# Kernel optimization log

Measured on AMD Instinct MI355X. Metric: run time of the kernel, lower is better.

The kernel has to match this reference:

```python
import jax, jax.numpy as jnp
import numpy as np

H = 300   # hidden_size
B = 2048  # number of graphs
L = 64    # max atoms per graph


def _ragged():
    sizes = 32 + (np.arange(B) % 33)          # sizes in [32, 64], deterministic
    starts = np.concatenate([[0], np.cumsum(sizes)[:-1]])
    N = int(sizes.sum())                       # 98273
    seg_id = np.repeat(np.arange(B), sizes)    # graph id per global node row
    offset = np.arange(N) - starts[seg_id]     # local position within graph
    return sizes, starts, N, seg_id, offset


def setup_inputs() -> dict:
    key = jax.random.key(0)
    sizes, starts, N, seg_id, offset = _ragged()
    ks = jax.random.split(key, 10)
    s = 1.0 / np.sqrt(H)
    u = lambda k, shp: jax.random.uniform(k, shp, jnp.float32, -s, s)
    return {
        "node": jax.random.normal(ks[0], (N, H), jnp.float32),
        "bias": u(ks[1], (H,)),
        "W_ih_f": u(ks[2], (3 * H, H)), "W_hh_f": u(ks[3], (3 * H, H)),
        "b_ih_f": u(ks[4], (3 * H,)), "b_hh_f": u(ks[5], (3 * H,)),
        "W_ih_b": u(ks[6], (3 * H, H)), "W_hh_b": u(ks[7], (3 * H, H)),
        "b_ih_b": u(ks[8], (3 * H,)), "b_hh_b": u(ks[9], (3 * H,)),
        "starts": jnp.asarray(starts, jnp.int32),
        "sizes": jnp.asarray(sizes, jnp.int32),
        "seg_id": jnp.asarray(seg_id, jnp.int32),
        "offset": jnp.asarray(offset, jnp.int32),
    }


def _gru_dir(x, h0, W_ih, W_hh, b_ih, b_hh, reverse):
    # x: [B, L, H], h0: [B, H]; torch nn.GRU cell math, one direction
    xp = jnp.einsum('blh,gh->blg', x, W_ih) + b_ih  # [B, L, 3H]

    def step(h, xt):
        gh = h @ W_hh.T + b_hh
        i_r, i_z, i_n = jnp.split(xt, 3, axis=-1)
        h_r, h_z, h_n = jnp.split(gh, 3, axis=-1)
        r = jax.nn.sigmoid(i_r + h_r)
        z = jax.nn.sigmoid(i_z + h_z)
        n = jnp.tanh(i_n + r * h_n)
        h_new = (1.0 - z) * n + z * h
        return h_new, h_new

    _, ys = jax.lax.scan(step, h0, jnp.swapaxes(xp, 0, 1), reverse=reverse)
    return jnp.swapaxes(ys, 0, 1)  # [B, L, H], time-aligned to input


def reference(node, bias, W_ih_f, W_hh_f, b_ih_f, b_hh_f,
              W_ih_b, W_hh_b, b_ih_b, b_hh_b,
              starts, sizes, seg_id, offset):
    N = node.shape[0]
    message = jax.nn.relu(node + bias)                       # [N, H]

    l_idx = jnp.arange(L)
    mask = l_idx[None, :] < sizes[:, None]                   # [B, L] valid positions
    idx = jnp.clip(starts[:, None] + l_idx[None, :], 0, N - 1)

    # pack: zero-padded per-graph message batch [B, L, H]
    padded = jnp.where(mask[..., None], message[idx], 0.0)
    # per-graph max-pool of raw hidden (node) -> h0 for both GRU directions
    hpool = jnp.max(jnp.where(mask[..., None], node[idx], -jnp.inf), axis=1)

    out_f = _gru_dir(padded, hpool, W_ih_f, W_hh_f, b_ih_f, b_hh_f, reverse=False)
    out_b = _gru_dir(padded, hpool, W_ih_b, W_hh_b, b_ih_b, b_hh_b, reverse=True)
    cur = jnp.concatenate([out_f, out_b], axis=-1)           # [B, L, 2H]

    # unpad back to flat node order
    unpad = cur[seg_id, offset]                              # [N, 2H]
    head = jnp.concatenate([message[:1], message[:1]], axis=1)  # [1, 2H]
    return jnp.concatenate([head, unpad], axis=0)            # [N+1, 2H]
```

## Files before the change

kernel.cpp:

```cpp
#include <hip/hip_runtime.h>
#include <math.h>

#define Hc 300
#define Ld 64
#define GB 16
#define GBF 16
#define KT 10
#define NQ 20
#define NT 60
#define PERDIR (2*2*KT*NT*64)
#define TOTF   (2*PERDIR)
#define NCW 10
#define NTH 768

typedef _Float16 f16x8 __attribute__((ext_vector_type(8)));
typedef float f32x4 __attribute__((ext_vector_type(4)));
typedef unsigned int u32;

#define MFMA16(a,b,c) __builtin_amdgcn_mfma_f32_16x16x32_f16(a,b,c,0,0,0)
#define RBAR() do { __builtin_amdgcn_sched_barrier(0); __builtin_amdgcn_s_barrier(); __builtin_amdgcn_sched_barrier(0); } while (0)

__global__ __launch_bounds__(256) void k_prep(
    const float* __restrict__ Wih_f, const float* __restrict__ Whh_f,
    const float* __restrict__ Wih_b, const float* __restrict__ Whh_b,
    const float* __restrict__ bih_f, const float* __restrict__ bhh_f,
    const float* __restrict__ bih_b, const float* __restrict__ bhh_b,
    const float* __restrict__ node, const float* __restrict__ bias,
    f16x8* __restrict__ Bfrag, float* __restrict__ bcomb, float* __restrict__ out)
{
  int gid = blockIdx.x*256 + threadIdx.x;
  if (gid < TOTF) {
    int lane = gid & 63;
    int s = gid >> 6;
    int nt = s % NT;  s /= NT;
    int kt = s % KT;  s /= KT;
    int term = s & 1; s >>= 1;
    int gemm = s & 1; s >>= 1;
    int dir  = s;
    int sec = nt / NQ, qq = nt - sec*NQ;
    int c = qq*16 + (lane & 15);
    int row = sec*Hc + c;
    const float* W = dir ? (gemm ? Whh_b : Wih_b) : (gemm ? Whh_f : Wih_f);
    f16x8 v;
#pragma unroll
    for (int e = 0; e < 8; ++e) {
      int k = kt*32 + (lane>>4)*8 + e;
      float wv = (c < Hc && k < Hc) ? W[row*Hc + k] : 0.f;
      _Float16 hi = (_Float16)wv;
      v[e] = term ? (_Float16)(wv - (float)hi) : hi;
    }
    Bfrag[gid] = v;
    return;
  }
  int i = gid - TOTF;
  if (i < 2560) {
    int dir = i / 1280; int r = i - dir*1280;
    int buf = r / 320, c = r - buf*320;
    const float* bih = dir ? bih_b : bih_f;
    const float* bhh = dir ? bhh_b : bhh_f;
    float v = 0.f;
    if (c < Hc) {
      if (buf == 0) v = bih[c] + bhh[c];
      else if (buf == 1) v = bih[Hc+c] + bhh[Hc+c];
      else if (buf == 2) v = bih[2*Hc+c];
      else v = bhh[2*Hc+c];
    }
    bcomb[i] = v;
    return;
  }
  i -= 2560;
  if (i < 600) {
    int c = (i < Hc) ? i : i - Hc;
    out[i] = fmaxf(node[c] + bias[c], 0.f);
  }
}

__device__ __forceinline__ u32 f32_to_hl(float v) {
  union { _Float16 f; unsigned short u; } a, b;
  a.f = (_Float16)v;
  b.f = (_Float16)(v - (float)a.f);
  return (u32)a.u | ((u32)b.u << 16);
}

__device__ __forceinline__ float ntl1(const float* p) {
  return __builtin_nontemporal_load(p);
}
__device__ __forceinline__ f32x4 ntl4(const float* p) {
  return __builtin_nontemporal_load((const f32x4*)p);
}

__device__ __forceinline__ void gll16(const void* g, void* l) {
  __builtin_amdgcn_global_load_lds(
      (const __attribute__((address_space(1))) u32*)g,
      (__attribute__((address_space(3))) u32*)l, 16, 0, 0);
}

__device__ __forceinline__ void afh_write(u32 (&buf)[2][KT][256],
                                          int l15, int g, int cE, u32 p, int lane) {
  u32 qv = (u32)__builtin_amdgcn_ds_bpermute((lane ^ 1) << 2, (int)p);
  int kt = cE >> 5;
  int dw = ((((cE >> 3) & 3) << 4) + g) * 4 + ((cE & 7) >> 1);
  if ((l15 & 1) == 0) buf[0][kt][dw] = (p & 0xFFFFu) | (qv << 16);
  else                buf[1][kt][dw] = (qv >> 16) | (p & 0xFFFF0000u);
}

__device__ __forceinline__ float sigf(float x) {
  return __builtin_amdgcn_rcpf(1.f + __expf(-x));
}
__device__ __forceinline__ float tanhfast(float x) {
  return 1.f - 2.f * __builtin_amdgcn_rcpf(__expf(2.f * x) + 1.f);
}

__global__ __launch_bounds__(640) void k_xp(
    const float* __restrict__ node, const float* __restrict__ bias,
    const f16x8* __restrict__ Bfrag, float* __restrict__ xp, int Nrows)
{
  __shared__ __align__(16) u32 AfX[2][4][KT][256];
  int tid = threadIdx.x, w = tid >> 6, lane = tid & 63;
  int l15 = lane & 15, l4 = lane >> 4;
  int r0 = blockIdx.x * 64;

  int k8 = w*32 + (l4 << 3);
  float bb[8];
#pragma unroll
  for (int e = 0; e < 8; ++e) bb[e] = 0.f;
  if (k8 + 8 <= Hc) {
    f32x4 a = *(const f32x4*)&bias[k8];
    f32x4 b = *(const f32x4*)&bias[k8+4];
#pragma unroll
    for (int e = 0; e < 4; ++e) { bb[e] = a[e]; bb[e+4] = b[e]; }
  } else if (k8 < Hc) {
    f32x4 a = *(const f32x4*)&bias[k8];
#pragma unroll
    for (int e = 0; e < 4; ++e) bb[e] = a[e];
  }

#pragma unroll
  for (int mt = 0; mt < 4; ++mt) {
    int row = r0 + mt*16 + l15;
    float xv[8];
#pragma unroll
    for (int e = 0; e < 8; ++e) xv[e] = 0.f;
    if (row < Nrows) {
      const float* rp = node + (size_t)row * Hc + k8;
      if (k8 + 8 <= Hc) {
        f32x4 a = ntl4(rp);
        f32x4 b = ntl4(rp + 4);
#pragma unroll
        for (int e = 0; e < 4; ++e) {
          xv[e]   = fmaxf(a[e] + bb[e],   0.f);
          xv[e+4] = fmaxf(b[e] + bb[e+4], 0.f);
        }
      } else if (k8 < Hc) {
        f32x4 a = ntl4(rp);
#pragma unroll
        for (int e = 0; e < 4; ++e) xv[e] = fmaxf(a[e] + bb[e], 0.f);
      }
    }
    f16x8 vh, vl;
#pragma unroll
    for (int e = 0; e < 8; ++e) {
      vh[e] = (_Float16)xv[e];
      vl[e] = (_Float16)(xv[e] - (float)vh[e]);
    }
    *(f16x8*)&AfX[0][mt][w][lane*4] = vh;
    *(f16x8*)&AfX[1][mt][w][lane*4] = vl;
  }
  __syncthreads();

  int qv0 = w, qv1 = w + 10;
  int c0 = qv0*16 + l15, c1 = qv1*16 + l15;
  const f32x4 zz = {0.f, 0.f, 0.f, 0.f};

#pragma unroll 1
  for (int dir = 0; dir < 2; ++dir) {
    const f16x8* Bxh = Bfrag + (size_t)dir * PERDIR;

#pragma unroll 1
    for (int qi = 0; qi < 2; ++qi) {
      int qv = qi ? qv1 : qv0;
      int c  = qi ? c1  : c0;
      f32x4 acc[3][4];
#pragma unroll
      for (int sec = 0; sec < 3; ++sec)
#pragma unroll
        for (int mt = 0; mt < 4; ++mt) acc[sec][mt] = zz;

#pragma unroll 2
      for (int kt = 0; kt < KT; ++kt) {
        f16x8 axh[4], axl[4];
#pragma unroll
        for (int mt = 0; mt < 4; ++mt) {
          axh[mt] = *(const f16x8*)&AfX[0][mt][kt][lane*4];
          axl[mt] = *(const f16x8*)&AfX[1][mt][kt][lane*4];
        }
#pragma unroll
        for (int sec = 0; sec < 3; ++sec) {
          int nt = sec*NQ + qv;
          f16x8 bh = Bxh[(kt*NT + nt)*64 + lane];
#pragma unroll
          for (int mt = 0; mt < 4; ++mt) {
            acc[sec][mt] = MFMA16(axh[mt], bh, acc[sec][mt]);
            acc[sec][mt] = MFMA16(axl[mt], bh, acc[sec][mt]);
          }
        }
      }
      if (c < 304) {
#pragma unroll
        for (int sec = 0; sec < 3; ++sec)
#pragma unroll
          for (int mt = 0; mt < 4; ++mt)
#pragma unroll
            for (int j = 0; j < 4; ++j) {
              int row = r0 + mt*16 + (l4<<2) + j;
              if (row < Nrows)
                __builtin_nontemporal_store(acc[sec][mt][j],
                    &xp[((size_t)row*2 + dir)*912 + sec*304 + c]);
            }
      }
    }
  }
}

__global__ __launch_bounds__(NTH) void k_rec(
    const float* __restrict__ node,
    const f16x8* __restrict__ Bfrag, const float* __restrict__ bcomb,
    const float* __restrict__ xp,
    const int* __restrict__ starts, const int* __restrict__ sizes,
    float* __restrict__ out)
{
  __shared__ __align__(16) u32 Bbuf[4][7680];
  __shared__ __align__(16) u32 AfH[2][KT][256];
  __shared__ int sst[16], ssz[16];

  int bid = blockIdx.x;
  int dir = (bid & 7) >= 4;
  int tslot = (bid & 3) + (bid >> 3) * 4;
  int g0 = tslot * GB;

  int tid = threadIdx.x;
  int w = tid >> 6, lane = tid & 63;
  int l15 = lane & 15, l4 = lane >> 4;

  if (tid < 16) { sst[tid] = starts[g0 + tid]; ssz[tid] = sizes[g0 + tid]; }

  const f16x8* Bhh = Bfrag + (size_t)dir * PERDIR + 2*KT*NT*64;
  const f32x4 zz = {0.f, 0.f, 0.f, 0.f};

  bool prod = (w >= NCW);
  int pw = w - NCW;

  int qv0 = w, qv1 = w + 10;
  int c0 = qv0*16 + l15, c1 = qv1*16 + l15;

  const float* bc = bcomb + dir*1280;
  float bcr[2], bcz[2], bci[2], bch[2];
  float hreg0[4], hreg1[4];

#define PISSUE(U) { \
    int kt_ = (U) >> 1, hf_ = (U) & 1; \
    char* sb_ = ((char*)&Bbuf[0][0]) + ((U) & 3) * 30720; \
    _Pragma("unroll") \
    for (int ff = 0; ff < 15; ++ff) { \
      int fi_ = pw*15 + ff; \
      int q3_ = fi_ / 3; \
      int sec_ = fi_ - 3*q3_; \
      const f16x8* gs_ = Bhh + ((size_t)(kt_*NT + sec_*NQ + hf_*10 + q3_))*64 + lane; \
      gll16((const void*)gs_, (void*)(sb_ + fi_*1024)); \
    } }

  if (prod) {
    PISSUE(0) PISSUE(1) PISSUE(2)
    asm volatile("s_waitcnt vmcnt(30)" ::: "memory");
  } else {
    bcr[0] = bc[c0];       bcr[1] = bc[c1];
    bcz[0] = bc[320 + c0]; bcz[1] = bc[320 + c1];
    bci[0] = bc[640 + c0]; bci[1] = bc[640 + c1];
    bch[0] = bc[960 + c0]; bch[1] = bc[960 + c1];
  }
  asm volatile("s_waitcnt lgkmcnt(0)" ::: "memory");
  RBAR();

  if (!prod) {
#pragma unroll
    for (int j = 0; j < 4; ++j) {
      int g = (l4<<2) + j;
      int st = sst[g], sz = ssz[g];
      float m0 = -1e30f, m1 = 0.f;
      for (int i = 0; i < sz; ++i)
        m0 = fmaxf(m0, ntl1(&node[(size_t)(st + i) * Hc + c0]));
      if (c1 < Hc) {
        m1 = -1e30f;
        for (int i = 0; i < sz; ++i)
          m1 = fmaxf(m1, ntl1(&node[(size_t)(st + i) * Hc + c1]));
      }
      hreg0[j] = m0;
      hreg1[j] = m1;
      afh_write(AfH, l15, g, c0 & ~1, f32_to_hl(m0), lane);
      afh_write(AfH, l15, g, c1 & ~1, f32_to_hl(m1), lane);
    }
  }
  asm volatile("s_waitcnt lgkmcnt(0)" ::: "memory");
  RBAR();

#pragma unroll 1
  for (int t = 0; t < Ld; ++t) {
    int time = dir ? (Ld-1-t) : t;

    float xvv0[3][4], xvv1[3][4];
    if (!prod) {
#pragma unroll
      for (int j = 0; j < 4; ++j) {
        int g = (l4<<2) + j;
        bool v = (time < ssz[g]);
        const float* xb = xp + ((size_t)(sst[g] + time)*2 + dir)*912 + c0;
#pragma unroll
        for (int sec = 0; sec < 3; ++sec)
          xvv0[sec][j] = v ? ntl1(xb + sec*304) : 0.f;
        bool v1 = (c1 < 304) && v;
        const float* xb1 = xp + ((size_t)(sst[g] + time)*2 + dir)*912 + c1;
#pragma unroll
        for (int sec = 0; sec < 3; ++sec)
          xvv1[sec][j] = v1 ? ntl1(xb1 + sec*304) : 0.f;
      }
    }

    f32x4 ha0[3] = { zz, zz, zz };
    f32x4 ha1[3] = { zz, zz, zz };

#pragma unroll 1
    for (int kt = 0; kt < KT; ++kt) {
      if (prod) {
        int u3 = 2*kt + 3; if (u3 >= 20) u3 -= 20;
        PISSUE(u3)
        asm volatile("s_waitcnt vmcnt(30)" ::: "memory");
      } else {
        const char* bbase = (const char*)&Bbuf[0][0] + ((2*kt) & 3)*30720 + lane*16;
        f16x8 ah = *(const f16x8*)&AfH[0][kt][lane*4];
        f16x8 al = *(const f16x8*)&AfH[1][kt][lane*4];
#pragma unroll
        for (int sec = 0; sec < 3; ++sec) {
          f16x8 b0 = *(const f16x8*)(bbase + (w*3 + sec)*1024);
          ha0[sec] = MFMA16(ah, b0, ha0[sec]);
          ha0[sec] = MFMA16(al, b0, ha0[sec]);
        }
      }
      RBAR();

      if (prod) {
        int u4 = 2*kt + 4; if (u4 >= 20) u4 -= 20;
        PISSUE(u4)
        asm volatile("s_waitcnt vmcnt(30)" ::: "memory");
      } else {
        const char* bbase = (const char*)&Bbuf[0][0] + ((2*kt+1) & 3)*30720 + lane*16;
        f16x8 ah = *(const f16x8*)&AfH[0][kt][lane*4];
        f16x8 al = *(const f16x8*)&AfH[1][kt][lane*4];
#pragma unroll
        for (int sec = 0; sec < 3; ++sec) {
          f16x8 b1 = *(const f16x8*)(bbase + (w*3 + sec)*1024);
          ha1[sec] = MFMA16(ah, b1, ha1[sec]);
          ha1[sec] = MFMA16(al, b1, ha1[sec]);
        }
      }
      RBAR();
    }

    if (!prod) {
#pragma unroll
      for (int j = 0; j < 4; ++j) {
        int g = (l4<<2) + j;
        float rr = sigf(ha0[0][j] + xvv0[0][j] + bcr[0]);
        float zi = sigf(ha0[1][j] + xvv0[1][j] + bcz[0]);
        float nn = tanhfast(xvv0[2][j] + bci[0] + rr * (ha0[2][j] + bch[0]));
        float h_ = (1.f - zi) * nn + zi * hreg0[j];
        hreg0[j] = h_;
        if (time < ssz[g])
          __builtin_nontemporal_store(h_,
              &out[(size_t)(1 + sst[g] + time)*600 + dir*Hc + c0]);
        afh_write(AfH, l15, g, c0 & ~1, f32_to_hl(h_), lane);

        float rr1 = sigf(ha1[0][j] + xvv1[0][j] + bcr[1]);
        float zi1 = sigf(ha1[1][j] + xvv1[1][j] + bcz[1]);
        float nn1 = tanhfast(xvv1[2][j] + bci[1] + rr1 * (ha1[2][j] + bch[1]));
        float h1 = (1.f - zi1) * nn1 + zi1 * hreg1[j];
        if (c1 >= Hc) h1 = 0.f;
        hreg1[j] = h1;
        if (c1 < Hc && time < ssz[g])
          __builtin_nontemporal_store(h1,
              &out[(size_t)(1 + sst[g] + time)*600 + dir*Hc + c1]);
        afh_write(AfH, l15, g, c1 & ~1, f32_to_hl(h1), lane);
      }
    }
    asm volatile("s_waitcnt lgkmcnt(0)" ::: "memory");
    RBAR();
  }
#undef PISSUE
}

__global__ __launch_bounds__(640) void k_rec_fb(
    const float* __restrict__ node, const float* __restrict__ bias,
    const f16x8* __restrict__ Bfrag, const float* __restrict__ bcomb,
    const int* __restrict__ starts, const int* __restrict__ sizes,
    float* __restrict__ out)
{
  __shared__ __align__(16) u32 AfX[2][4][KT][256];
  __shared__ __align__(16) u32 AfH[2][2][KT][256];
  __shared__ int sst[GBF], ssz[GBF];

  int bid = blockIdx.x;
  int dir = (bid & 7) >= 4;
  int tslot = (bid & 3) + (bid >> 3) * 4;
  int g0 = tslot * GBF;

  int tid = threadIdx.x;
  int w = tid >> 6, lane = tid & 63;
  int l15 = lane & 15, l4 = lane >> 4;

  if (tid < GBF) { sst[tid] = starts[g0 + tid]; ssz[tid] = sizes[g0 + tid]; }
  __syncthreads();

  int qv[2] = { w, w + 10 };
  int cq[2] = { qv[0]*16 + l15, qv[1]*16 + l15 };

  const float* bc = bcomb + dir*1280;
  float bcr[2], bcz[2], bci[2], bch[2];
#pragma unroll
  for (int qi = 0; qi < 2; ++qi) {
    int c = cq[qi];
    bcr[qi] = bc[c]; bcz[qi] = bc[320 + c]; bci[qi] = bc[640 + c]; bch[qi] = bc[960 + c];
  }
  int stj[4], szj[4];
#pragma unroll
  for (int j = 0; j < 4; ++j) { stj[j] = sst[(l4<<2)+j]; szj[j] = ssz[(l4<<2)+j]; }
  int stG = sst[l15], szG = ssz[l15];

  const f16x8* Bd  = Bfrag + (size_t)dir * PERDIR;
  const f16x8* Bxh = Bd;
  const f16x8* Bxl = Bd + KT*NT*64;
  const f16x8* Bhh = Bd + 2*KT*NT*64;
  const f16x8* Bhl = Bd + 3*KT*NT*64;
  const f32x4 zz = {0.f, 0.f, 0.f, 0.f};

  int k8 = w*32 + (l4<<3);
  float bb[8];
#pragma unroll
  for (int e = 0; e < 8; ++e) bb[e] = 0.f;
  if (k8 + 8 <= Hc) {
    f32x4 a = *(const f32x4*)&bias[k8];
    f32x4 b = *(const f32x4*)&bias[k8+4];
#pragma unroll
    for (int e = 0; e < 4; ++e) { bb[e] = a[e]; bb[e+4] = b[e]; }
  } else if (k8 < Hc) {
    f32x4 a = *(const f32x4*)&bias[k8];
#pragma unroll
    for (int e = 0; e < 4; ++e) bb[e] = a[e];
  }

  float hreg[2][4];
#pragma unroll
  for (int qi = 0; qi < 2; ++qi) {
    int c = cq[qi];
#pragma unroll
    for (int j = 0; j < 4; ++j) {
      float m = 0.f;
      if (c < Hc) {
        m = -1e30f;
        int st = stj[j], sz = szj[j];
        for (int i = 0; i < sz; ++i)
          m = fmaxf(m, node[(size_t)(st + i) * Hc + c]);
      }
      hreg[qi][j] = m;
      afh_write(AfH[0], l15, (l4<<2)+j, c & ~1, f32_to_hl(m), lane);
    }
  }

#define HSTEPF(S) { \
    constexpr int CUR = (S)&1; \
    constexpr int NXT = CUR^1; \
    f32x4 ha[2][3]; \
    _Pragma("unroll") \
    for (int qi = 0; qi < 2; ++qi) { ha[qi][0] = zz; ha[qi][1] = zz; ha[qi][2] = zz; } \
    _Pragma("unroll 2") \
    for (int kt = 0; kt < KT; ++kt) { \
      f16x8 ahh = *(const f16x8*)&AfH[CUR][0][kt][lane*4]; \
      f16x8 ahl = *(const f16x8*)&AfH[CUR][1][kt][lane*4]; \
      _Pragma("unroll") \
      for (int qi = 0; qi < 2; ++qi) { \
        _Pragma("unroll") \
        for (int sec = 0; sec < 3; ++sec) { \
          int nt = sec*NQ + qv[qi]; \
          f16x8 bh = Bhh[(kt*NT + nt)*64 + lane]; \
          f16x8 bl = Bhl[(kt*NT + nt)*64 + lane]; \
          ha[qi][sec] = MFMA16(ahh, bh, ha[qi][sec]); \
          ha[qi][sec] = MFMA16(ahh, bl, ha[qi][sec]); \
          ha[qi][sec] = MFMA16(ahl, bh, ha[qi][sec]); \
        } \
      } \
    } \
    int tt = 4*T + (S); \
    int time = dir ? (Ld-1-tt) : tt; \
    _Pragma("unroll") \
    for (int qi = 0; qi < 2; ++qi) { \
      int c = cq[qi]; \
      _Pragma("unroll") \
      for (int j = 0; j < 4; ++j) { \
        float rp_ = ha[qi][0][j] + xa[qi][0][S][j] + bcr[qi]; \
        float zp_ = ha[qi][1][j] + xa[qi][1][S][j] + bcz[qi]; \
        float r_ = 1.f/(1.f + __expf(-rp_)); \
        float z_ = 1.f/(1.f + __expf(-zp_)); \
        float n_ = tanhf(xa[qi][2][S][j] + bci[qi] + r_*(ha[qi][2][j] + bch[qi])); \
        float h_ = (1.f - z_)*n_ + z_*hreg[qi][j]; \
        if (c >= Hc) h_ = 0.f; \
        hreg[qi][j] = h_; \
        if (c < Hc && time < szj[j]) \
          out[(size_t)(1 + stj[j] + time)*600 + dir*Hc + c] = h_; \
        afh_write(AfH[NXT], l15, (l4<<2)+j, c & ~1, f32_to_hl(h_), lane); \
      } \
    } \
    __syncthreads(); \
  }

#pragma unroll 1
  for (int T = 0; T < Ld/4; ++T) {
#pragma unroll
    for (int s = 0; s < 4; ++s) {
      int tt = 4*T + s;
      int time = dir ? (Ld-1-tt) : tt;
      float xv[8];
#pragma unroll
      for (int e = 0; e < 8; ++e) xv[e] = 0.f;
      if (time < szG) {
        const float* rp = node + (size_t)(stG + time) * Hc + k8;
        if (k8 + 8 <= Hc) {
          f32x4 a = *(const f32x4*)rp;
          f32x4 b = *(const f32x4*)(rp + 4);
#pragma unroll
          for (int e = 0; e < 4; ++e) {
            xv[e]   = fmaxf(a[e] + bb[e],   0.f);
            xv[e+4] = fmaxf(b[e] + bb[e+4], 0.f);
          }
        } else if (k8 < Hc) {
          f32x4 a = *(const f32x4*)rp;
#pragma unroll
          for (int e = 0; e < 4; ++e) xv[e] = fmaxf(a[e] + bb[e], 0.f);
        }
      }
      f16x8 vh, vl;
#pragma unroll
      for (int e = 0; e < 8; ++e) {
        vh[e] = (_Float16)xv[e];
        vl[e] = (_Float16)(xv[e] - (float)vh[e]);
      }
      *(f16x8*)&AfX[0][s][w][lane*4] = vh;
      *(f16x8*)&AfX[1][s][w][lane*4] = vl;
    }
    __syncthreads();

    f32x4 xa[2][3][4];
#pragma unroll
    for (int qi = 0; qi < 2; ++qi)
#pragma unroll
      for (int sec = 0; sec < 3; ++sec)
#pragma unroll
        for (int mt = 0; mt < 4; ++mt) xa[qi][sec][mt] = zz;

#pragma unroll 1
    for (int kt = 0; kt < KT; ++kt) {
      f16x8 axh[4], axl[4];
#pragma unroll
      for (int mt = 0; mt < 4; ++mt) {
        axh[mt] = *(const f16x8*)&AfX[0][mt][kt][lane*4];
        axl[mt] = *(const f16x8*)&AfX[1][mt][kt][lane*4];
      }
#pragma unroll
      for (int qi = 0; qi < 2; ++qi) {
#pragma unroll
        for (int sec = 0; sec < 3; ++sec) {
          int nt = sec*NQ + qv[qi];
          f16x8 bh = Bxh[(kt*NT + nt)*64 + lane];
          f16x8 bl = Bxl[(kt*NT + nt)*64 + lane];
#pragma unroll
          for (int mt = 0; mt < 4; ++mt) {
            xa[qi][sec][mt] = MFMA16(axh[mt], bh, xa[qi][sec][mt]);
            xa[qi][sec][mt] = MFMA16(axh[mt], bl, xa[qi][sec][mt]);
            xa[qi][sec][mt] = MFMA16(axl[mt], bh, xa[qi][sec][mt]);
          }
        }
      }
    }

    HSTEPF(0)
    HSTEPF(1)
    HSTEPF(2)
    HSTEPF(3)
  }
#undef HSTEPF
}

extern "C" void kernel_launch(void* const* d_in, const int* in_sizes, int n_in,
                              void* d_out, int out_size, void* d_ws, size_t ws_size,
                              hipStream_t stream) {
  const float* node  = (const float*)d_in[0];
  const float* bias  = (const float*)d_in[1];
  const float* Wih_f = (const float*)d_in[2];
  const float* Whh_f = (const float*)d_in[3];
  const float* bih_f = (const float*)d_in[4];
  const float* bhh_f = (const float*)d_in[5];
  const float* Wih_b = (const float*)d_in[6];
  const float* Whh_b = (const float*)d_in[7];
  const float* bih_b = (const float*)d_in[8];
  const float* bhh_b = (const float*)d_in[9];
  const int* starts  = (const int*)d_in[10];
  const int* sizes   = (const int*)d_in[11];

  int ngr = in_sizes[10];
  int N = in_sizes[0] / Hc;

  float* out = (float*)d_out;
  f16x8* Bfrag = (f16x8*)d_ws;
  float* bcomb = (float*)((char*)d_ws + (size_t)TOTF*16);
  size_t xp_off = (size_t)TOTF*16 + 2560*4;
  size_t need = xp_off + (size_t)N * 1824 * 4;

  int prep_threads = TOTF + 2560 + 600;
  hipLaunchKernelGGL(k_prep, dim3((prep_threads + 255)/256), dim3(256), 0, stream,
                     Wih_f, Whh_f, Wih_b, Whh_b, bih_f, bhh_f, bih_b, bhh_b,
                     node, bias, Bfrag, bcomb, out);

  if (ws_size >= need && (ngr % GB) == 0) {
    float* xp = (float*)((char*)d_ws + xp_off);
    int nxb = (N + 63) / 64;
    hipLaunchKernelGGL(k_xp, dim3(nxb), dim3(640), 0, stream,
                       node, bias, Bfrag, xp, N);
    int ntile = ngr / GB;
    hipLaunchKernelGGL(k_rec, dim3(2*ntile), dim3(NTH), 0, stream,
                       node, Bfrag, bcomb, xp, starts, sizes, out);
  } else {
    int ntilef = ngr / GBF;
    hipLaunchKernelGGL(k_rec_fb, dim3(2*ntilef), dim3(640), 0, stream,
                       node, bias, Bfrag, bcomb, starts, sizes, out);
  }
}
```

Baseline: 1.365 ms.

## Restructure recurrent weight streaming into a 7-slot per-gate ring buffer

The W_hh streaming in the recurrent kernel moves from 4 half-k-tile buffers to a 7-slot ring with one slot per gate section of a k-tile, so 30 sub-waves run per timestep instead of 20. Each slot holds only the 19 column quads that are actually needed, which skips loading and multiplying the padded 20th quad. The producer waves keep more loads in flight (up to 6 slots ahead) with per-wave vmcnt thresholds. The cost is more barriers per timestep and tighter coupling to exact vmcnt counts.

```diff
diff --git a/kernel.cpp b/kernel.cpp
--- a/kernel.cpp
+++ b/kernel.cpp
@@ -12,6 +12,8 @@
 #define TOTF   (2*PERDIR)
 #define NCW 10
 #define NTH 768
+#define NSL 7
+#define SLOTB 19456
 
 typedef _Float16 f16x8 __attribute__((ext_vector_type(8)));
 typedef float f32x4 __attribute__((ext_vector_type(4)));
@@ -229,7 +231,7 @@
     const int* __restrict__ starts, const int* __restrict__ sizes,
     float* __restrict__ out)
 {
-  __shared__ __align__(16) u32 Bbuf[4][7680];
+  __shared__ __align__(16) u32 ring[NSL*4864];
   __shared__ __align__(16) u32 AfH[2][KT][256];
   __shared__ int sst[16], ssz[16];
 
@@ -249,6 +251,7 @@
 
   bool prod = (w >= NCW);
   int pw = w - NCW;
+  int qb = pw ? 10 : 0;
 
   int qv0 = w, qv1 = w + 10;
   int c0 = qv0*16 + l15, c1 = qv1*16 + l15;
@@ -257,21 +260,25 @@
   float bcr[2], bcz[2], bci[2], bch[2];
   float hreg0[4], hreg1[4];
 
-#define PISSUE(U) { \
-    int kt_ = (U) >> 1, hf_ = (U) & 1; \
-    char* sb_ = ((char*)&Bbuf[0][0]) + ((U) & 3) * 30720; \
+#define PISSUE(KT_, SEC_, WS_) { \
+    char* sb_ = (char*)ring + (WS_)*SLOTB; \
     _Pragma("unroll") \
-    for (int ff = 0; ff < 15; ++ff) { \
-      int fi_ = pw*15 + ff; \
-      int q3_ = fi_ / 3; \
-      int sec_ = fi_ - 3*q3_; \
-      const f16x8* gs_ = Bhh + ((size_t)(kt_*NT + sec_*NQ + hf_*10 + q3_))*64 + lane; \
-      gll16((const void*)gs_, (void*)(sb_ + fi_*1024)); \
+    for (int ff = 0; ff < 10; ++ff) { \
+      int q_ = qb + ff; \
+      if (q_ < 19) { \
+        const f16x8* gs_ = Bhh + ((size_t)((KT_)*NT + (SEC_)*NQ + q_))*64 + lane; \
+        gll16((const void*)gs_, (void*)(sb_ + q_*1024)); \
+      } \
     } }
 
+#define PWAIT() { \
+    if (pw == 0) asm volatile("s_waitcnt vmcnt(50)" ::: "memory"); \
+    else         asm volatile("s_waitcnt vmcnt(45)" ::: "memory"); }
+
   if (prod) {
-    PISSUE(0) PISSUE(1) PISSUE(2)
-    asm volatile("s_waitcnt vmcnt(30)" ::: "memory");
+    PISSUE(0, 0, 0) PISSUE(0, 1, 1) PISSUE(0, 2, 2)
+    PISSUE(1, 0, 3) PISSUE(1, 1, 4) PISSUE(1, 2, 5)
+    PWAIT()
   } else {
     bcr[0] = bc[c0];       bcr[1] = bc[c1];
     bcz[0] = bc[320 + c0]; bcz[1] = bc[320 + c1];
@@ -303,6 +310,34 @@
   asm volatile("s_waitcnt lgkmcnt(0)" ::: "memory");
   RBAR();
 
+  int rs = 0;
+  int ws = 6;
+  int ktp = 2;
+
+#define SUBW(SEC) { \
+    if (prod) { \
+      PISSUE(ktp, SEC, ws) \
+      PWAIT() \
+    } else { \
+      if ((SEC) == 0) { \
+        ah = *(const f16x8*)&AfH[0][kt][lane*4]; \
+        al = *(const f16x8*)&AfH[1][kt][lane*4]; \
+      } \
+      const char* bb_ = (const char*)ring + rs*SLOTB + lane*16; \
+      f16x8 b0_ = *(const f16x8*)(bb_ + qv0*1024); \
+      ha0[SEC] = MFMA16(ah, b0_, ha0[SEC]); \
+      ha0[SEC] = MFMA16(al, b0_, ha0[SEC]); \
+      if (qv1 < 19) { \
+        f16x8 b1_ = *(const f16x8*)(bb_ + qv1*1024); \
+        ha1[SEC] = MFMA16(ah, b1_, ha1[SEC]); \
+        ha1[SEC] = MFMA16(al, b1_, ha1[SEC]); \
+      } \
+    } \
+    RBAR(); \
+    rs = (rs == NSL-1) ? 0 : rs + 1; \
+    ws = (ws == NSL-1) ? 0 : ws + 1; \
+  }
+
 #pragma unroll 1
   for (int t = 0; t < Ld; ++t) {
     int time = dir ? (Ld-1-t) : t;
@@ -330,39 +365,11 @@
 
 #pragma unroll 1
     for (int kt = 0; kt < KT; ++kt) {
-      if (prod) {
-        int u3 = 2*kt + 3; if (u3 >= 20) u3 -= 20;
-        PISSUE(u3)
-        asm volatile("s_waitcnt vmcnt(30)" ::: "memory");
-      } else {
-        const char* bbase = (const char*)&Bbuf[0][0] + ((2*kt) & 3)*30720 + lane*16;
-        f16x8 ah = *(const f16x8*)&AfH[0][kt][lane*4];
-        f16x8 al = *(const f16x8*)&AfH[1][kt][lane*4];
-#pragma unroll
-        for (int sec = 0; sec < 3; ++sec) {
-          f16x8 b0 = *(const f16x8*)(bbase + (w*3 + sec)*1024);
-          ha0[sec] = MFMA16(ah, b0, ha0[sec]);
-          ha0[sec] = MFMA16(al, b0, ha0[sec]);
-        }
-      }
-      RBAR();
-
-      if (prod) {
-        int u4 = 2*kt + 4; if (u4 >= 20) u4 -= 20;
-        PISSUE(u4)
-        asm volatile("s_waitcnt vmcnt(30)" ::: "memory");
-      } else {
-        const char* bbase = (const char*)&Bbuf[0][0] + ((2*kt+1) & 3)*30720 + lane*16;
-        f16x8 ah = *(const f16x8*)&AfH[0][kt][lane*4];
-        f16x8 al = *(const f16x8*)&AfH[1][kt][lane*4];
-#pragma unroll
-        for (int sec = 0; sec < 3; ++sec) {
-          f16x8 b1 = *(const f16x8*)(bbase + (w*3 + sec)*1024);
-          ha1[sec] = MFMA16(ah, b1, ha1[sec]);
-          ha1[sec] = MFMA16(al, b1, ha1[sec]);
-        }
-      }
-      RBAR();
+      f16x8 ah, al;
+      SUBW(0)
+      SUBW(1)
+      SUBW(2)
+      ktp = (ktp == KT-1) ? 0 : ktp + 1;
     }
 
     if (!prod) {
@@ -394,7 +401,11 @@
     asm volatile("s_waitcnt lgkmcnt(0)" ::: "memory");
     RBAR();
   }
+
+  if (prod) asm volatile("s_waitcnt vmcnt(0)" ::: "memory");
+#undef SUBW
 #undef PISSUE
+#undef PWAIT
 }
 
 __global__ __launch_bounds__(640) void k_rec_fb(
```

Result: slower. 1.441 ms (+5.6%).
